# Optimization experiments

Hardware: AMD Instinct MI355X
Metric: run time of the kernel (lower is better)

Reference implementation:

```python
import jax, jax.numpy as jnp
import numpy as np

K = 3          # deformable conv kernel size
PAD = 1        # padding
BN_EPS = 1e-5


def _upsample2(x):
    # nn.Upsample(scale_factor=2) default mode='nearest' on [B,C,D,H,W]
    x = jnp.repeat(x, 2, axis=2)
    x = jnp.repeat(x, 2, axis=3)
    x = jnp.repeat(x, 2, axis=4)
    return x


def _conv3d(x, w, b):
    out = jax.lax.conv_general_dilated(
        x, w, window_strides=(1, 1, 1), padding=[(PAD, PAD)] * 3,
        dimension_numbers=('NCDHW', 'OIDHW', 'NCDHW'))
    return out + b[None, :, None, None, None]


def _trilinear_sample(x, coords):
    # x: [B,C,D,H,W]; coords: [B,Kt,3,D,H,W] absolute (possibly OOB) positions.
    # Zero padding outside the volume (standard deformable-conv convention).
    B, C, D, H, W = x.shape
    pd, ph, pw = coords[:, :, 0], coords[:, :, 1], coords[:, :, 2]  # [B,Kt,D,H,W]
    d0 = jnp.floor(pd); h0 = jnp.floor(ph); w0 = jnp.floor(pw)
    fd = pd - d0; fh = ph - h0; fw = pw - w0
    x_flat = x.reshape(B, C, D * H * W)

    def gather(di, hi, wi):
        valid = ((di >= 0) & (di < D) & (hi >= 0) & (hi < H) & (wi >= 0) & (wi < W))
        dc = jnp.clip(di, 0, D - 1).astype(jnp.int32)
        hc = jnp.clip(hi, 0, H - 1).astype(jnp.int32)
        wc = jnp.clip(wi, 0, W - 1).astype(jnp.int32)
        flat = (dc * H + hc) * W + wc                       # [B,Kt,D,H,W]
        vals = jax.vmap(lambda xf, idx: jnp.take(xf, idx.reshape(-1), axis=1))(x_flat, flat)
        vals = vals.reshape(B, C, *flat.shape[1:])          # [B,C,Kt,D,H,W]
        return vals * valid[:, None].astype(x.dtype)

    out = jnp.zeros((B, C) + pd.shape[1:], x.dtype)
    for dd in (0, 1):
        for hh in (0, 1):
            for ww in (0, 1):
                wgt = ((fd if dd else 1.0 - fd)
                       * (fh if hh else 1.0 - fh)
                       * (fw if ww else 1.0 - fw))           # [B,Kt,D,H,W]
                out = out + gather(d0 + dd, h0 + hh, w0 + ww) * wgt[:, None]
    return out  # [B,C,Kt,D,H,W]


def _deform_conv3d(x, w_off, b_off, w, b):
    B, C, D, H, W = x.shape
    Kt = K ** 3
    # offsets: Conv3d(C, 3*K^3, k=3, pad=1) -> [B, Kt, 3(dz,dy,dx), D,H,W]
    off = _conv3d(x, w_off, b_off).reshape(B, Kt, 3, D, H, W)
    # kernel tap displacements relative to output voxel: [Kt,3]
    taps = jnp.stack(jnp.meshgrid(jnp.arange(K), jnp.arange(K), jnp.arange(K),
                                  indexing='ij'), -1).reshape(-1, 3).astype(x.dtype) - PAD
    grid = jnp.stack(jnp.meshgrid(jnp.arange(D, dtype=x.dtype),
                                  jnp.arange(H, dtype=x.dtype),
                                  jnp.arange(W, dtype=x.dtype),
                                  indexing='ij'), 0)          # [3,D,H,W]
    coords = grid[None, None] + taps[None, :, :, None, None, None] + off  # [B,Kt,3,D,H,W]
    sampled = _trilinear_sample(x, coords)                    # [B,C,Kt,D,H,W]
    out = jnp.einsum('bckdhw,ock->bodhw', sampled, w.reshape(w.shape[0], C, Kt))
    return out + b[None, :, None, None, None]


def setup_inputs() -> dict:
    key = jax.random.key(0)
    ks = jax.random.split(key, 4)
    ch_in, ch_out = 64, 32
    x = jax.random.normal(ks[0], (1, ch_in, 16, 16, 16), jnp.float32)
    w_off = jax.random.normal(ks[1], (3 * K ** 3, ch_in, K, K, K), jnp.float32) * 0.01
    b_off = jnp.zeros((3 * K ** 3,), jnp.float32)
    w = jax.random.normal(ks[2], (ch_out, ch_in, K, K, K), jnp.float32) * 0.05
    b = jnp.zeros((ch_out,), jnp.float32)
    gamma = jnp.ones((ch_out,), jnp.float32)
    beta = jnp.zeros((ch_out,), jnp.float32)
    return {"x": x, "w_off": w_off, "b_off": b_off, "w": w, "b": b,
            "gamma": gamma, "beta": beta}


def reference(x, w_off, b_off, w, b, gamma, beta):
    x = _upsample2(x)                                  # [B,C,2D,2H,2W]
    out = _deform_conv3d(x, w_off, b_off, w, b)        # [B,ch_out,2D,2H,2W]
    # BatchNorm3d (training-mode batch stats) + ReLU
    mean = out.mean(axis=(0, 2, 3, 4), keepdims=True)
    var = out.var(axis=(0, 2, 3, 4), keepdims=True)
    out = (out - mean) * jax.lax.rsqrt(var + BN_EPS)
    out = out * gamma[None, :, None, None, None] + beta[None, :, None, None, None]
    return jax.nn.relu(out)
```

## Files before the change

### kernel.cpp

```cpp
#include <hip/hip_runtime.h>
#include <math.h>

#define NVOX  32768
#define CIN   64
#define COUT  32
#define KT    27
#define CIT   1728
#define PSP   5832

#define WS_XT   0
#define WS_WA   186624
#define WS_WO   214272
#define WS_STAT 297216

#define SST 584

typedef __attribute__((ext_vector_type(8))) _Float16 half8;
typedef __attribute__((ext_vector_type(2))) _Float16 half2v;
typedef __attribute__((ext_vector_type(4))) float floatx4;

static __device__ __forceinline__ unsigned dup16(float w) {
    unsigned short b = __builtin_bit_cast(unsigned short, (_Float16)w);
    return (unsigned)b * 0x10001u;
}
static __device__ __forceinline__ half2v u2h2(unsigned u) {
    return __builtin_bit_cast(half2v, u);
}

__global__ __launch_bounds__(256) void prep_all_kernel(
        const float* __restrict__ x, const float* __restrict__ w_off,
        const float* __restrict__ wmat, float* __restrict__ ws) {
    int b = blockIdx.x, t = threadIdx.x;
    if (b < 92) {
        __shared__ _Float16 tile[64][65];
        _Float16* xth = (_Float16*)(ws + WS_XT);
        int tq = t >> 6, lane = t & 63;
        int base = b * 64;
        int cell = base + lane;
        int qw = cell % 18, qh = (cell / 18) % 18, qd = cell / 324;
        bool interior = (cell < PSP) && qd >= 1 && qd <= 16 && qh >= 1 && qh <= 16
                        && qw >= 1 && qw <= 16;
        int xbase = interior ? (((qd - 1) * 16 + (qh - 1)) * 16 + (qw - 1)) : 0;
#pragma unroll
        for (int i = 0; i < 16; i++) {
            int c = tq * 16 + i;
            float v = interior ? x[c * 4096 + xbase] : 0.f;
            tile[lane][c] = (_Float16)v;
        }
        __syncthreads();
#pragma unroll
        for (int i = 0; i < 16; i++) {
            int s = tq * 16 + i;
            int cell2 = base + s;
            if (cell2 < PSP) xth[cell2 * 64 + lane] = tile[s][lane];
        }
    } else if (b < 119) {
        _Float16* wa = (_Float16*)(ws + WS_WA);
        int idx = (b - 92) * 256 + t;
        int kb = idx >> 5, o = idx & 31;
        half8 r;
#pragma unroll
        for (int j = 0; j < 8; j++) {
            int kk = kb * 8 + j;
            int tap = kk >> 6, ci = kk & 63;
            r[j] = (_Float16)wmat[o * CIT + ci * 27 + tap];
        }
        *(half8*)(wa + idx * 8) = r;
    } else if (b < 200) {
        _Float16* wo = (_Float16*)(ws + WS_WO);
        int idx = (b - 119) * 256 + t;
        int kb = idx / 96, m = idx % 96;
        half8 r;
#pragma unroll
        for (int j = 0; j < 8; j++) {
            int kk = kb * 8 + j;
            int tap = kk >> 6, ci = kk & 63;
            float v = (m < 81) ? w_off[(m * 64 + ci) * 27 + tap] : 0.f;
            r[j] = (_Float16)v;
        }
        *(half8*)(wo + idx * 8) = r;
    } else {
        if (t < 64) ws[WS_STAT + t] = 0.f;
    }
}

__global__ __launch_bounds__(256) void deform_kernel(
        const float* __restrict__ b_off, const float* __restrict__ bias,
        float* ws, float* __restrict__ out) {
    __shared__ __align__(16) unsigned short smem[16 * SST];
    __shared__ __align__(16) _Float16 Plh[81 * 16];
    __shared__ __align__(16) char ubuf[9216];
    __shared__ float rsum[COUT], rsq[COUT];

    float*    red  = (float*)ubuf;
    int*      cba  = (int*)ubuf;
    unsigned* cbw  = (unsigned*)(ubuf + 4608);
    float*    pbuf = (float*)ubuf;

    const half2v* xt2 = (const half2v*)(ws + WS_XT);
    const unsigned* xtu = (const unsigned*)(ws + WS_XT);
    const half8* wa8 = (const half8*)(ws + WS_WA);
    const half8* wo8 = (const half8*)(ws + WS_WO);
    float* gstat = ws + WS_STAT;

    int tid = threadIdx.x, wave = tid >> 6, lane = tid & 63;
    int vsel = lane >> 5, cl = lane & 31;
    int pbase = blockIdx.x * 16;
    int d = pbase >> 10, h = (pbase >> 5) & 31, w0 = pbase & 31;

    if (tid < COUT) { rsum[tid] = 0.f; rsq[tid] = 0.f; }

    int mh = wave & 1, kh = wave >> 1;
    int col = lane & 15, quad = lane >> 4;

    floatx4 oacc0 = {0.f,0.f,0.f,0.f}, oacc1 = {0.f,0.f,0.f,0.f}, oacc2 = {0.f,0.f,0.f,0.f};
#pragma unroll 1
    for (int g = 0; g < 3; g++) {
        if (g) __syncthreads();
        int rd = ((d + g - 1) >> 1) + 1;
#pragma unroll
        for (int tl = 0; tl < 9; tl++) {
            int kh2 = tl / 3, kw2 = tl % 3;
            int rh = ((h + kh2 - 1) >> 1) + 1;
#pragma unroll
            for (int pi = 0; pi < 2; pi++) {
                int v = wave * 4 + pi * 2 + vsel;
                int w = w0 + v;
                int rw = ((w + kw2 - 1) >> 1) + 1;
                int cell = (rd * 18 + rh) * 18 + rw;
                unsigned uv = xtu[cell * 32 + cl];
                *(unsigned*)(smem + v * SST + tl * 64 + 2 * cl) = uv;
            }
        }
        __syncthreads();
#pragma unroll
        for (int s = 0; s < 9; s++) {
            int k_local = kh * 288 + s * 32;
            int kb = ((g * 576 + k_local) >> 3) + quad;
            half8 bfrag = *(const half8*)(smem + col * SST + k_local + quad * 8);
            half8 a0 = wo8[kb * 96 + mh * 48 + col];
            half8 a1 = wo8[kb * 96 + mh * 48 + 16 + col];
            half8 a2 = wo8[kb * 96 + mh * 48 + 32 + col];
            oacc0 = __builtin_amdgcn_mfma_f32_16x16x32_f16(a0, bfrag, oacc0, 0, 0, 0);
            oacc1 = __builtin_amdgcn_mfma_f32_16x16x32_f16(a1, bfrag, oacc1, 0, 0, 0);
            oacc2 = __builtin_amdgcn_mfma_f32_16x16x32_f16(a2, bfrag, oacc2, 0, 0, 0);
        }
    }
    __syncthreads();
    if (kh == 1) {
#pragma unroll
        for (int r = 0; r < 4; r++) {
            red[(mh * 48 +      quad * 4 + r) * 16 + col] = oacc0[r];
            red[(mh * 48 + 16 + quad * 4 + r) * 16 + col] = oacc1[r];
            red[(mh * 48 + 32 + quad * 4 + r) * 16 + col] = oacc2[r];
        }
    }
    __syncthreads();
    if (kh == 0) {
#pragma unroll
        for (int r = 0; r < 4; r++) {
            int m0 = mh * 48 + quad * 4 + r;
            Plh[m0 * 16 + col] = (_Float16)(oacc0[r] + red[m0 * 16 + col] + b_off[m0]);
            int m1 = m0 + 16;
            Plh[m1 * 16 + col] = (_Float16)(oacc1[r] + red[m1 * 16 + col] + b_off[m1]);
            int m2 = m0 + 32;
            if (m2 < 81)
                Plh[m2 * 16 + col] = (_Float16)(oacc2[r] + red[m2 * 16 + col] + b_off[m2]);
        }
    }

    int mt = wave & 1;
    floatx4 acc = {0.f, 0.f, 0.f, 0.f};

#pragma unroll 1
    for (int g = 0; g < 3; g++) {
        __syncthreads();
        if (tid < 144) {
            int v = tid & 15, tl = tid >> 4;
            int tap = g * 9 + tl;
            int kh2 = tl / 3, kw2 = tl % 3;
            int w = w0 + v;
            float od = (float)Plh[(3 * tap + 0) * 16 + v];
            float oh = (float)Plh[(3 * tap + 1) * 16 + v];
            float ow = (float)Plh[(3 * tap + 2) * 16 + v];
            float pdc = (float)(d + g - 1) + od;
            float phc = (float)(h + kh2 - 1) + oh;
            float pwc = (float)(w + kw2 - 1) + ow;
            float fd0 = floorf(pdc), fh0 = floorf(phc), fw0 = floorf(pwc);
            float fd = pdc - fd0, fh = phc - fh0, fw = pwc - fw0;
            int id = (int)fd0, ih = (int)fh0, iw = (int)fw0;
            int rd0 = ((min(max(id,     -2), 33) >> 1) + 1) * (324 * 32);
            int rd1 = ((min(max(id + 1, -2), 33) >> 1) + 1) * (324 * 32);
            int rh0 = ((min(max(ih,     -2), 33) >> 1) + 1) * (18 * 32);
            int rh1 = ((min(max(ih + 1, -2), 33) >> 1) + 1) * (18 * 32);
            int rw0 = ((min(max(iw,     -2), 33) >> 1) + 1) * 32;
            int rw1 = ((min(max(iw + 1, -2), 33) >> 1) + 1) * 32;
            int* A = cba + tid * 8;
            unsigned* W = cbw + tid * 8;
            A[0] = rd0 + rh0 + rw0; A[1] = rd0 + rh0 + rw1;
            A[2] = rd0 + rh1 + rw0; A[3] = rd0 + rh1 + rw1;
            A[4] = rd1 + rh0 + rw0; A[5] = rd1 + rh0 + rw1;
            A[6] = rd1 + rh1 + rw0; A[7] = rd1 + rh1 + rw1;
            float gd = 1.f - fd, gh = 1.f - fh, gw = 1.f - fw;
            W[0] = dup16(gd * gh * gw); W[1] = dup16(gd * gh * fw);
            W[2] = dup16(gd * fh * gw); W[3] = dup16(gd * fh * fw);
            W[4] = dup16(fd * gh * gw); W[5] = dup16(fd * gh * fw);
            W[6] = dup16(fd * fh * gw); W[7] = dup16(fd * fh * fw);
        }
        __syncthreads();

#pragma unroll
        for (int tl = 0; tl < 9; tl++) {
#pragma unroll
            for (int pi = 0; pi < 2; pi++) {
                int v = wave * 4 + pi * 2 + vsel;
                int item = tl * 16 + v;
                const int4* a4 = (const int4*)(cba + item * 8);
                const int4* w4 = (const int4*)(cbw + item * 8);
                int4 A0 = a4[0], A1 = a4[1];
                int4 U0 = w4[0], U1 = w4[1];
                half2v s = u2h2(U0.x) * xt2[A0.x + cl];
                s += u2h2(U0.y) * xt2[A0.y + cl];
                s += u2h2(U0.z) * xt2[A0.z + cl];
                s += u2h2(U0.w) * xt2[A0.w + cl];
                s += u2h2(U1.x) * xt2[A1.x + cl];
                s += u2h2(U1.y) * xt2[A1.y + cl];
                s += u2h2(U1.z) * xt2[A1.z + cl];
                s += u2h2(U1.w) * xt2[A1.w + cl];
                *(unsigned*)(smem + v * SST + tl * 64 + 2 * cl) =
                    __builtin_bit_cast(unsigned, s);
            }
        }
        __syncthreads();

#pragma unroll
        for (int s = 0; s < 9; s++) {
            int k_local = kh * 288 + s * 32;
            int kb = ((g * 576 + k_local) >> 3) + quad;
            half8 afrag = wa8[kb * 32 + mt * 16 + col];
            half8 bfrag = *(const half8*)(smem + col * SST + k_local + quad * 8);
            acc = __builtin_amdgcn_mfma_f32_16x16x32_f16(afrag, bfrag, acc, 0, 0, 0);
        }
    }
    __syncthreads();

    if (kh == 1) {
#pragma unroll
        for (int r = 0; r < 4; r++) pbuf[mt * 256 + (quad * 4 + r) * 16 + col] = acc[r];
    }
    __syncthreads();
    if (kh == 0) {
#pragma unroll
        for (int r = 0; r < 4; r++) {
            int o = mt * 16 + quad * 4 + r;
            float val = acc[r] + pbuf[mt * 256 + (quad * 4 + r) * 16 + col] + bias[o];
            out[o * NVOX + pbase + col] = val;
            atomicAdd(&rsum[o], val);
            atomicAdd(&rsq[o], val * val);
        }
    }
    __syncthreads();
    if (tid < COUT) {
        atomicAdd(&gstat[tid], rsum[tid]);
        atomicAdd(&gstat[COUT + tid], rsq[tid]);
    }
}

__global__ void bn_kernel(const float* __restrict__ ws,
                          const float* __restrict__ gamma,
                          const float* __restrict__ beta,
                          float* out) {
    int i = blockIdx.x * 256 + threadIdx.x;
    int o = i >> 15;
    const float* gstat = ws + WS_STAT;
    const float inv = 1.f / 32768.f;
    float mean = gstat[o] * inv;
    float var  = gstat[COUT + o] * inv - mean * mean;
    float sc   = rsqrtf(var + 1e-5f) * gamma[o];
    float v = (out[i] - mean) * sc + beta[o];
    out[i] = fmaxf(v, 0.f);
}

extern "C" void kernel_launch(void* const* d_in, const int* in_sizes, int n_in,
                              void* d_out, int out_size, void* d_ws, size_t ws_size,
                              hipStream_t stream) {
    const float* x     = (const float*)d_in[0];
    const float* w_off = (const float*)d_in[1];
    const float* b_off = (const float*)d_in[2];
    const float* wmat  = (const float*)d_in[3];
    const float* bias  = (const float*)d_in[4];
    const float* gamma = (const float*)d_in[5];
    const float* beta  = (const float*)d_in[6];
    float* ws  = (float*)d_ws;
    float* out = (float*)d_out;

    prep_all_kernel<<<201, 256, 0, stream>>>(x, w_off, wmat, ws);
    deform_kernel<<<2048, 256, 0, stream>>>(b_off, bias, ws, out);
    bn_kernel<<<4096, 256, 0, stream>>>(ws, gamma, beta, out);
}
```

Measured before the change: 165.0 us.

## Split offset conv into separate kernel and gather directly into MFMA registers

Moves the offset convolution into its own kernel that streams the offset weights through a double-buffered LDS tile, with each block covering a 32-voxel row, and writes fp16 offsets to a workspace buffer. The deform kernel now computes sampling coordinates per lane and builds the MFMA B fragments directly in registers from 16-byte gathers. This removes the LDS staging and most of the barriers. The two wave pairs split the taps instead of the K range. This adds an extra kernel launch and a global round trip for the offsets, and raises per-thread register pressure.

Measured after the change: 211.8 us. 1.28x slower.

```diff
diff --git a/kernel.cpp b/kernel.cpp
--- a/kernel.cpp
+++ b/kernel.cpp
@@ -12,8 +12,7 @@
 #define WS_WA   186624
 #define WS_WO   214272
 #define WS_STAT 297216
-
-#define SST 584
+#define WS_P    297280
 
 typedef __attribute__((ext_vector_type(8))) _Float16 half8;
 typedef __attribute__((ext_vector_type(2))) _Float16 half2v;
@@ -25,6 +24,11 @@
 }
 static __device__ __forceinline__ half2v u2h2(unsigned u) {
     return __builtin_bit_cast(half2v, u);
+}
+static __device__ __forceinline__ half8 pk8(half2v a, half2v b, half2v c, half2v d) {
+    union { half8 v; half2v p[4]; } u;
+    u.p[0] = a; u.p[1] = b; u.p[2] = c; u.p[3] = d;
+    return u.v;
 }
 
 __global__ __launch_bounds__(256) void prep_all_kernel(
@@ -84,179 +88,178 @@
     }
 }
 
-__global__ __launch_bounds__(256) void deform_kernel(
-        const float* __restrict__ b_off, const float* __restrict__ bias,
-        float* ws, float* __restrict__ out) {
-    __shared__ __align__(16) unsigned short smem[16 * SST];
-    __shared__ __align__(16) _Float16 Plh[81 * 16];
-    __shared__ __align__(16) char ubuf[9216];
+__global__ __launch_bounds__(256, 4) void offset_kernel(
+        const float* __restrict__ b_off, float* ws) {
+    __shared__ __align__(16) _Float16 abuf[2 * 6144];
+    int tid = threadIdx.x, wave = tid >> 6, lane = tid & 63;
+    int nsub = wave & 1, kh = wave >> 1;
+    int col = lane & 15, quad = lane >> 4;
+    int pbase = blockIdx.x * 32;
+    int d = blockIdx.x >> 5, h = blockIdx.x & 31;
+    int vox = nsub * 16 + col;
+    const char* xtb = (const char*)(ws + WS_XT);
+    const int4* wsrc = (const int4*)(ws + WS_WO);
+    _Float16* Pw = (_Float16*)(ws + WS_P);
+    int4* ab4 = (int4*)abuf;
+
+    int4 ra0 = wsrc[tid], ra1 = wsrc[256 + tid], ra2 = wsrc[512 + tid];
+    ab4[tid] = ra0; ab4[256 + tid] = ra1; ab4[512 + tid] = ra2;
+    ra0 = wsrc[768 + tid]; ra1 = wsrc[768 + 256 + tid]; ra2 = wsrc[768 + 512 + tid];
+    __syncthreads();
+
+    floatx4 acc[6];
+#pragma unroll
+    for (int mt = 0; mt < 6; mt++) acc[mt] = (floatx4){0.f, 0.f, 0.f, 0.f};
+
+    int fb = (kh * 4 + quad) * 768 + col * 8;
+
+#pragma unroll 1
+    for (int tap = 0; tap < 27; tap++) {
+        if (tap < 26) {
+            int4* dst = ab4 + ((tap + 1) & 1) * 768;
+            dst[tid] = ra0; dst[256 + tid] = ra1; dst[512 + tid] = ra2;
+        }
+        if (tap < 25) {
+            const int4* s = wsrc + (tap + 2) * 768;
+            ra0 = s[tid]; ra1 = s[256 + tid]; ra2 = s[512 + tid];
+        }
+        int kd = tap / 9, r9 = tap - kd * 9, kh2 = r9 / 3, kw2 = r9 - kh2 * 3;
+        int rd = ((d + kd - 1) >> 1) + 1;
+        int rh = ((h + kh2 - 1) >> 1) + 1;
+        int rw = ((vox + kw2 - 1) >> 1) + 1;
+        int cell = (rd * 18 + rh) * 18 + rw;
+        int4 bx = *(const int4*)(xtb + cell * 128 + kh * 64 + quad * 16);
+        half8 bfrag = __builtin_bit_cast(half8, bx);
+        const _Float16* abh = abuf + (tap & 1) * 6144;
+#pragma unroll
+        for (int mt = 0; mt < 6; mt++) {
+            half8 af = *(const half8*)(abh + fb + mt * 128);
+            acc[mt] = __builtin_amdgcn_mfma_f32_16x16x32_f16(af, bfrag, acc[mt], 0, 0, 0);
+        }
+        __syncthreads();
+    }
+
+    float* red = (float*)abuf;
+    if (kh == 1) {
+#pragma unroll
+        for (int mt = 0; mt < 6; mt++)
+#pragma unroll
+            for (int r = 0; r < 4; r++)
+                red[(nsub * 96 + mt * 16 + quad * 4 + r) * 17 + col] = acc[mt][r];
+    }
+    __syncthreads();
+    if (kh == 0) {
+#pragma unroll
+        for (int mt = 0; mt < 6; mt++)
+#pragma unroll
+            for (int r = 0; r < 4; r++) {
+                int m = mt * 16 + quad * 4 + r;
+                if (m < 81) {
+                    float v = acc[mt][r] + red[(nsub * 96 + m) * 17 + col] + b_off[m];
+                    Pw[m * NVOX + pbase + nsub * 16 + col] = (_Float16)v;
+                }
+            }
+    }
+}
+
+#define GATH(Ax, Wx) do { \
+    int4 x0_ = *(const int4*)(xtb + (Ax) + sub); \
+    int4 x1_ = *(const int4*)(xtb + (Ax) + sub + 64); \
+    s00 += (Wx) * u2h2((unsigned)x0_.x); s01 += (Wx) * u2h2((unsigned)x0_.y); \
+    s02 += (Wx) * u2h2((unsigned)x0_.z); s03 += (Wx) * u2h2((unsigned)x0_.w); \
+    s10 += (Wx) * u2h2((unsigned)x1_.x); s11 += (Wx) * u2h2((unsigned)x1_.y); \
+    s12 += (Wx) * u2h2((unsigned)x1_.z); s13 += (Wx) * u2h2((unsigned)x1_.w); \
+} while (0)
+
+__global__ __launch_bounds__(256, 4) void deform_kernel(
+        const float* __restrict__ bias, float* ws, float* __restrict__ out) {
+    __shared__ float pbuf[2][2][16][17];
     __shared__ float rsum[COUT], rsq[COUT];
-
-    float*    red  = (float*)ubuf;
-    int*      cba  = (int*)ubuf;
-    unsigned* cbw  = (unsigned*)(ubuf + 4608);
-    float*    pbuf = (float*)ubuf;
-
-    const half2v* xt2 = (const half2v*)(ws + WS_XT);
-    const unsigned* xtu = (const unsigned*)(ws + WS_XT);
+    int tid = threadIdx.x, wave = tid >> 6, lane = tid & 63;
+    int nsub = wave & 1, kt = wave >> 1;
+    int col = lane & 15, quad = lane >> 4;
+    int pbase = blockIdx.x * 32;
+    int d = blockIdx.x >> 5, h = blockIdx.x & 31;
+    int vox = nsub * 16 + col;
+    int gvox = pbase + vox;
+    const char* xtb = (const char*)(ws + WS_XT);
     const half8* wa8 = (const half8*)(ws + WS_WA);
-    const half8* wo8 = (const half8*)(ws + WS_WO);
+    const _Float16* P = (const _Float16*)(ws + WS_P);
     float* gstat = ws + WS_STAT;
 
-    int tid = threadIdx.x, wave = tid >> 6, lane = tid & 63;
-    int vsel = lane >> 5, cl = lane & 31;
-    int pbase = blockIdx.x * 16;
-    int d = pbase >> 10, h = (pbase >> 5) & 31, w0 = pbase & 31;
-
     if (tid < COUT) { rsum[tid] = 0.f; rsq[tid] = 0.f; }
 
-    int mh = wave & 1, kh = wave >> 1;
-    int col = lane & 15, quad = lane >> 4;
-
-    floatx4 oacc0 = {0.f,0.f,0.f,0.f}, oacc1 = {0.f,0.f,0.f,0.f}, oacc2 = {0.f,0.f,0.f,0.f};
+    floatx4 acc0 = {0.f, 0.f, 0.f, 0.f}, acc1 = {0.f, 0.f, 0.f, 0.f};
+    int tbeg = kt ? 14 : 0, tend = kt ? 27 : 14;
+    int sub = quad * 16;
+
 #pragma unroll 1
-    for (int g = 0; g < 3; g++) {
-        if (g) __syncthreads();
-        int rd = ((d + g - 1) >> 1) + 1;
-#pragma unroll
-        for (int tl = 0; tl < 9; tl++) {
-            int kh2 = tl / 3, kw2 = tl % 3;
-            int rh = ((h + kh2 - 1) >> 1) + 1;
-#pragma unroll
-            for (int pi = 0; pi < 2; pi++) {
-                int v = wave * 4 + pi * 2 + vsel;
-                int w = w0 + v;
-                int rw = ((w + kw2 - 1) >> 1) + 1;
-                int cell = (rd * 18 + rh) * 18 + rw;
-                unsigned uv = xtu[cell * 32 + cl];
-                *(unsigned*)(smem + v * SST + tl * 64 + 2 * cl) = uv;
-            }
-        }
-        __syncthreads();
-#pragma unroll
-        for (int s = 0; s < 9; s++) {
-            int k_local = kh * 288 + s * 32;
-            int kb = ((g * 576 + k_local) >> 3) + quad;
-            half8 bfrag = *(const half8*)(smem + col * SST + k_local + quad * 8);
-            half8 a0 = wo8[kb * 96 + mh * 48 + col];
-            half8 a1 = wo8[kb * 96 + mh * 48 + 16 + col];
-            half8 a2 = wo8[kb * 96 + mh * 48 + 32 + col];
-            oacc0 = __builtin_amdgcn_mfma_f32_16x16x32_f16(a0, bfrag, oacc0, 0, 0, 0);
-            oacc1 = __builtin_amdgcn_mfma_f32_16x16x32_f16(a1, bfrag, oacc1, 0, 0, 0);
-            oacc2 = __builtin_amdgcn_mfma_f32_16x16x32_f16(a2, bfrag, oacc2, 0, 0, 0);
-        }
-    }
-    __syncthreads();
-    if (kh == 1) {
+    for (int tap = tbeg; tap < tend; tap++) {
+        int kd = tap / 9, r9 = tap - kd * 9, kh2 = r9 / 3, kw2 = r9 - kh2 * 3;
+        float od = (float)P[(3 * tap + 0) * NVOX + gvox];
+        float oh = (float)P[(3 * tap + 1) * NVOX + gvox];
+        float ow = (float)P[(3 * tap + 2) * NVOX + gvox];
+        float pdc = (float)(d + kd - 1) + od;
+        float phc = (float)(h + kh2 - 1) + oh;
+        float pwc = (float)(vox + kw2 - 1) + ow;
+        float fd0 = floorf(pdc), fh0 = floorf(phc), fw0 = floorf(pwc);
+        float fd = pdc - fd0, fh = phc - fh0, fw = pwc - fw0;
+        int id = (int)fd0, ih = (int)fh0, iw = (int)fw0;
+        int rd0 = ((min(max(id,     -2), 33) >> 1) + 1) * (324 * 128);
+        int rd1 = ((min(max(id + 1, -2), 33) >> 1) + 1) * (324 * 128);
+        int rh0 = ((min(max(ih,     -2), 33) >> 1) + 1) * (18 * 128);
+        int rh1 = ((min(max(ih + 1, -2), 33) >> 1) + 1) * (18 * 128);
+        int rw0 = ((min(max(iw,     -2), 33) >> 1) + 1) * 128;
+        int rw1 = ((min(max(iw + 1, -2), 33) >> 1) + 1) * 128;
+        int A0 = rd0 + rh0 + rw0, A1 = rd0 + rh0 + rw1;
+        int A2 = rd0 + rh1 + rw0, A3 = rd0 + rh1 + rw1;
+        int A4 = rd1 + rh0 + rw0, A5 = rd1 + rh0 + rw1;
+        int A6 = rd1 + rh1 + rw0, A7 = rd1 + rh1 + rw1;
+        float gd = 1.f - fd, gh = 1.f - fh, gw = 1.f - fw;
+        half2v W0 = u2h2(dup16(gd * gh * gw)), W1 = u2h2(dup16(gd * gh * fw));
+        half2v W2 = u2h2(dup16(gd * fh * gw)), W3 = u2h2(dup16(gd * fh * fw));
+        half2v W4 = u2h2(dup16(fd * gh * gw)), W5 = u2h2(dup16(fd * gh * fw));
+        half2v W6 = u2h2(dup16(fd * fh * gw)), W7 = u2h2(dup16(fd * fh * fw));
+
+        half2v s00 = {0, 0}, s01 = {0, 0}, s02 = {0, 0}, s03 = {0, 0};
+        half2v s10 = {0, 0}, s11 = {0, 0}, s12 = {0, 0}, s13 = {0, 0};
+        GATH(A0, W0); GATH(A1, W1); GATH(A2, W2); GATH(A3, W3);
+        GATH(A4, W4); GATH(A5, W5); GATH(A6, W6); GATH(A7, W7);
+        half8 bf0 = pk8(s00, s01, s02, s03);
+        half8 bf1 = pk8(s10, s11, s12, s13);
+
+        int kb = tap * 8 + quad;
+        half8 a00 = wa8[kb * 32 + col];
+        half8 a01 = wa8[kb * 32 + 16 + col];
+        half8 a10 = wa8[(kb + 4) * 32 + col];
+        half8 a11 = wa8[(kb + 4) * 32 + 16 + col];
+        acc0 = __builtin_amdgcn_mfma_f32_16x16x32_f16(a00, bf0, acc0, 0, 0, 0);
+        acc1 = __builtin_amdgcn_mfma_f32_16x16x32_f16(a01, bf0, acc1, 0, 0, 0);
+        acc0 = __builtin_amdgcn_mfma_f32_16x16x32_f16(a10, bf1, acc0, 0, 0, 0);
+        acc1 = __builtin_amdgcn_mfma_f32_16x16x32_f16(a11, bf1, acc1, 0, 0, 0);
+    }
+    __syncthreads();
+    if (kt == 1) {
 #pragma unroll
         for (int r = 0; r < 4; r++) {
-            red[(mh * 48 +      quad * 4 + r) * 16 + col] = oacc0[r];
-            red[(mh * 48 + 16 + quad * 4 + r) * 16 + col] = oacc1[r];
-            red[(mh * 48 + 32 + quad * 4 + r) * 16 + col] = oacc2[r];
-        }
-    }
-    __syncthreads();
-    if (kh == 0) {
+            pbuf[nsub][0][quad * 4 + r][col] = acc0[r];
+            pbuf[nsub][1][quad * 4 + r][col] = acc1[r];
+        }
+    }
+    __syncthreads();
+    if (kt == 0) {
 #pragma unroll
         for (int r = 0; r < 4; r++) {
-            int m0 = mh * 48 + quad * 4 + r;
-            Plh[m0 * 16 + col] = (_Float16)(oacc0[r] + red[m0 * 16 + col] + b_off[m0]);
-            int m1 = m0 + 16;
-            Plh[m1 * 16 + col] = (_Float16)(oacc1[r] + red[m1 * 16 + col] + b_off[m1]);
-            int m2 = m0 + 32;
-            if (m2 < 81)
-                Plh[m2 * 16 + col] = (_Float16)(oacc2[r] + red[m2 * 16 + col] + b_off[m2]);
-        }
-    }
-
-    int mt = wave & 1;
-    floatx4 acc = {0.f, 0.f, 0.f, 0.f};
-
-#pragma unroll 1
-    for (int g = 0; g < 3; g++) {
-        __syncthreads();
-        if (tid < 144) {
-            int v = tid & 15, tl = tid >> 4;
-            int tap = g * 9 + tl;
-            int kh2 = tl / 3, kw2 = tl % 3;
-            int w = w0 + v;
-            float od = (float)Plh[(3 * tap + 0) * 16 + v];
-            float oh = (float)Plh[(3 * tap + 1) * 16 + v];
-            float ow = (float)Plh[(3 * tap + 2) * 16 + v];
-            float pdc = (float)(d + g - 1) + od;
-            float phc = (float)(h + kh2 - 1) + oh;
-            float pwc = (float)(w + kw2 - 1) + ow;
-            float fd0 = floorf(pdc), fh0 = floorf(phc), fw0 = floorf(pwc);
-            float fd = pdc - fd0, fh = phc - fh0, fw = pwc - fw0;
-            int id = (int)fd0, ih = (int)fh0, iw = (int)fw0;
-            int rd0 = ((min(max(id,     -2), 33) >> 1) + 1) * (324 * 32);
-            int rd1 = ((min(max(id + 1, -2), 33) >> 1) + 1) * (324 * 32);
-            int rh0 = ((min(max(ih,     -2), 33) >> 1) + 1) * (18 * 32);
-            int rh1 = ((min(max(ih + 1, -2), 33) >> 1) + 1) * (18 * 32);
-            int rw0 = ((min(max(iw,     -2), 33) >> 1) + 1) * 32;
-            int rw1 = ((min(max(iw + 1, -2), 33) >> 1) + 1) * 32;
-            int* A = cba + tid * 8;
-            unsigned* W = cbw + tid * 8;
-            A[0] = rd0 + rh0 + rw0; A[1] = rd0 + rh0 + rw1;
-            A[2] = rd0 + rh1 + rw0; A[3] = rd0 + rh1 + rw1;
-            A[4] = rd1 + rh0 + rw0; A[5] = rd1 + rh0 + rw1;
-            A[6] = rd1 + rh1 + rw0; A[7] = rd1 + rh1 + rw1;
-            float gd = 1.f - fd, gh = 1.f - fh, gw = 1.f - fw;
-            W[0] = dup16(gd * gh * gw); W[1] = dup16(gd * gh * fw);
-            W[2] = dup16(gd * fh * gw); W[3] = dup16(gd * fh * fw);
-            W[4] = dup16(fd * gh * gw); W[5] = dup16(fd * gh * fw);
-            W[6] = dup16(fd * fh * gw); W[7] = dup16(fd * fh * fw);
-        }
-        __syncthreads();
-
-#pragma unroll
-        for (int tl = 0; tl < 9; tl++) {
-#pragma unroll
-            for (int pi = 0; pi < 2; pi++) {
-                int v = wave * 4 + pi * 2 + vsel;
-                int item = tl * 16 + v;
-                const int4* a4 = (const int4*)(cba + item * 8);
-                const int4* w4 = (const int4*)(cbw + item * 8);
-                int4 A0 = a4[0], A1 = a4[1];
-                int4 U0 = w4[0], U1 = w4[1];
-                half2v s = u2h2(U0.x) * xt2[A0.x + cl];
-                s += u2h2(U0.y) * xt2[A0.y + cl];
-                s += u2h2(U0.z) * xt2[A0.z + cl];
-                s += u2h2(U0.w) * xt2[A0.w + cl];
-                s += u2h2(U1.x) * xt2[A1.x + cl];
-                s += u2h2(U1.y) * xt2[A1.y + cl];
-                s += u2h2(U1.z) * xt2[A1.z + cl];
-                s += u2h2(U1.w) * xt2[A1.w + cl];
-                *(unsigned*)(smem + v * SST + tl * 64 + 2 * cl) =
-                    __builtin_bit_cast(unsigned, s);
-            }
-        }
-        __syncthreads();
-
-#pragma unroll
-        for (int s = 0; s < 9; s++) {
-            int k_local = kh * 288 + s * 32;
-            int kb = ((g * 576 + k_local) >> 3) + quad;
-            half8 afrag = wa8[kb * 32 + mt * 16 + col];
-            half8 bfrag = *(const half8*)(smem + col * SST + k_local + quad * 8);
-            acc = __builtin_amdgcn_mfma_f32_16x16x32_f16(afrag, bfrag, acc, 0, 0, 0);
-        }
-    }
-    __syncthreads();
-
-    if (kh == 1) {
-#pragma unroll
-        for (int r = 0; r < 4; r++) pbuf[mt * 256 + (quad * 4 + r) * 16 + col] = acc[r];
-    }
-    __syncthreads();
-    if (kh == 0) {
-#pragma unroll
-        for (int r = 0; r < 4; r++) {
-            int o = mt * 16 + quad * 4 + r;
-            float val = acc[r] + pbuf[mt * 256 + (quad * 4 + r) * 16 + col] + bias[o];
-            out[o * NVOX + pbase + col] = val;
-            atomicAdd(&rsum[o], val);
-            atomicAdd(&rsq[o], val * val);
+            int o0 = quad * 4 + r;
+            float v0 = acc0[r] + pbuf[nsub][0][quad * 4 + r][col] + bias[o0];
+            out[o0 * NVOX + gvox] = v0;
+            atomicAdd(&rsum[o0], v0);
+            atomicAdd(&rsq[o0], v0 * v0);
+            int o1 = 16 + quad * 4 + r;
+            float v1 = acc1[r] + pbuf[nsub][1][quad * 4 + r][col] + bias[o1];
+            out[o1 * NVOX + gvox] = v1;
+            atomicAdd(&rsum[o1], v1);
+            atomicAdd(&rsq[o1], v1 * v1);
         }
     }
     __syncthreads();
@@ -295,6 +298,7 @@
     float* out = (float*)d_out;
 
     prep_all_kernel<<<201, 256, 0, stream>>>(x, w_off, wmat, ws);
-    deform_kernel<<<2048, 256, 0, stream>>>(b_off, bias, ws, out);
+    offset_kernel<<<1024, 256, 0, stream>>>(b_off, ws);
+    deform_kernel<<<1024, 256, 0, stream>>>(bias, ws, out);
     bn_kernel<<<4096, 256, 0, stream>>>(ws, gamma, beta, out);
 }
```
